# Performance work log

Hardware: AMD Instinct MI355X
Metric: run time of the kernel (lower is better)

The kernel has to match this reference:

```python
import jax, jax.numpy as jnp
import numpy as np

B, S, D_MODEL, D_K, D_V = 4, 2048, 1024, 1024, 1024


def setup_inputs() -> dict:
    key = jax.random.key(0)
    k1, k2, k3, k4 = jax.random.split(key, 4)
    scale = 1.0 / np.sqrt(D_MODEL)
    x = jax.random.normal(k1, (B, S, D_MODEL), dtype=jnp.float32)
    Wq = jax.random.normal(k2, (D_K, D_MODEL), dtype=jnp.float32) * scale
    Wk = jax.random.normal(k3, (D_K, D_MODEL), dtype=jnp.float32) * scale
    Wv = jax.random.normal(k4, (D_V, D_MODEL), dtype=jnp.float32) * scale
    # causal mask: position i may attend to j <= i (True = keep)
    mask = jnp.broadcast_to(jnp.tril(jnp.ones((S, S), dtype=bool)), (B, S, S))
    return {"x": x, "mask": mask, "Wq": Wq, "Wk": Wk, "Wv": Wv}


def reference(x, mask, Wq, Wk, Wv):
    # nn.Linear(d, k, bias=False): y = x @ W.T with W of shape [k, d]
    q = jnp.einsum('bsd,kd->bsk', x, Wq)
    k = jnp.einsum('bsd,kd->bsk', x, Wk)
    v = jnp.einsum('bsd,vd->bsv', x, Wv)
    scores = jnp.einsum('bik,bjk->bij', q, k) / jnp.sqrt(jnp.float32(D_K))
    s = jnp.where(mask, scores, -jnp.inf)
    # masked, fully-masked-row-safe softmax (fully masked rows -> all zeros,
    # matching softmax[all-masked rows] = 0 in the original)
    m = jnp.max(s, axis=-1, keepdims=True)
    m_safe = jnp.where(jnp.isfinite(m), m, 0.0)
    e = jnp.exp(s - m_safe)          # exp(-inf) = 0 for masked entries
    denom = jnp.sum(e, axis=-1, keepdims=True)
    p = e / jnp.where(denom == 0.0, 1.0, denom)
    return jnp.einsum('bij,bjv->biv', p, v)
```

## Files before the change

kernel.cpp:

```cpp
#include <hip/hip_runtime.h>
#include <hip/hip_bf16.h>
#include <stdint.h>

#define SEQ   2048
#define DM    1024
#define NBAT  4

typedef __attribute__((ext_vector_type(8))) short  short8;
typedef __attribute__((ext_vector_type(4))) float  floatx4;

__device__ __forceinline__ unsigned short f2b(float f) {
    __hip_bfloat16 h = __float2bfloat16(f);
    unsigned short r;
    __builtin_memcpy(&r, &h, 2);
    return r;
}

__device__ __forceinline__ ushort4 pack4(float a, float b, float c, float d) {
    ushort4 u; u.x = f2b(a); u.y = f2b(b); u.z = f2b(c); u.w = f2b(d); return u;
}

__device__ __forceinline__ void gload16(const void* g, void* s) {
    __builtin_amdgcn_global_load_lds(
        (const __attribute__((address_space(1))) unsigned int*)(uintptr_t)g,
        (__attribute__((address_space(3))) unsigned int*)(uintptr_t)s,
        16, 0, 0);
}

__global__ void prep(const float4* __restrict__ x,
                     const float4* __restrict__ w0, const float4* __restrict__ w1,
                     const float4* __restrict__ w2,
                     ushort4* __restrict__ xb, ushort4* __restrict__ wall,
                     float* __restrict__ rsum)
{
    const int b = blockIdx.x;
    const int t = threadIdx.x;
    if (b < 8192) {
        const int i = b * 256 + t;
        float4 f = x[i];
        xb[i] = pack4(f.x, f.y, f.z, f.w);
    } else if (b < 11264) {
        const int idx  = b - 8192;
        const int wsel = idx >> 10;
        const int i    = (idx & 1023) * 256 + t;
        const float4* src = (wsel == 0) ? w0 : (wsel == 1) ? w1 : w2;
        float4 f = src[i];
        wall[(size_t)wsel * 262144 + i] = pack4(f.x, f.y, f.z, f.w);
    } else {
        rsum[(b - 11264) * 256 + t] = 0.f;
    }
}

#define SLOTS 24576

__global__ __launch_bounds__(512, 2) void qkv_gemm(
    const unsigned short* __restrict__ A, const unsigned short* __restrict__ Bm,
    unsigned short* __restrict__ Qo, unsigned short* __restrict__ Ko,
    unsigned short* __restrict__ Vto, float qscale)
{
    __shared__ __align__(16) unsigned short lds[3 * SLOTS];

    const int bid = blockIdx.x;
    const int wg  = (bid & 7) * 96 + (bid >> 3);
    const int mt  = wg / 24, nt = wg - mt * 24;
    const int m0  = mt * 256, n0 = nt * 128;

    const int t    = threadIdx.x;
    const int w    = t >> 6;
    const int lane = t & 63;
    const int wr   = w >> 1, wc = w & 1;
    const int r    = lane & 15, q = lane >> 4;

    const int srow = lane >> 3;
    const int scol = ((lane & 7) ^ srow) << 3;

    const int aoff = (wr >> 1) * 8192 + ((wr & 1) * 64 + r) * 64;
    const int boff = 16384 + (wc * 64 + r) * 64;
    const int sk0  = ((0 + q) ^ (r & 7)) * 8;
    const int sk1  = ((4 + q) ^ (r & 7)) * 8;

    floatx4 acc[4][4];
#pragma unroll
    for (int i = 0; i < 4; i++)
#pragma unroll
        for (int j = 0; j < 4; j++)
            acc[i][j] = (floatx4){0.f, 0.f, 0.f, 0.f};

#define STGA(KB, SL) do { \
    gload16(A + (((size_t)(m0 +       w * 16 + srow)) << 10) + (KB) + scol, &lds[(SL) +         w * 1024]); \
    gload16(A + (((size_t)(m0 +   8 + w * 16 + srow)) << 10) + (KB) + scol, &lds[(SL) +         w * 1024 + 512]); \
    gload16(A + (((size_t)(m0 + 128 + w * 16 + srow)) << 10) + (KB) + scol, &lds[(SL) + 8192 +  w * 1024]); \
    gload16(A + (((size_t)(m0 + 136 + w * 16 + srow)) << 10) + (KB) + scol, &lds[(SL) + 8192 +  w * 1024 + 512]); \
  } while (0)
#define STGB(KB, SL) do { \
    gload16(Bm + (((size_t)(n0 +      w * 16 + srow)) << 10) + (KB) + scol, &lds[(SL) + 16384 + w * 1024]); \
    gload16(Bm + (((size_t)(n0 +  8 + w * 16 + srow)) << 10) + (KB) + scol, &lds[(SL) + 16384 + w * 1024 + 512]); \
  } while (0)

#define MFMA16() do { \
    acc[0][0] = __builtin_amdgcn_mfma_f32_16x16x32_bf16(af0, bf0, acc[0][0], 0, 0, 0); \
    acc[0][1] = __builtin_amdgcn_mfma_f32_16x16x32_bf16(af0, bf1, acc[0][1], 0, 0, 0); \
    acc[0][2] = __builtin_amdgcn_mfma_f32_16x16x32_bf16(af0, bf2, acc[0][2], 0, 0, 0); \
    acc[0][3] = __builtin_amdgcn_mfma_f32_16x16x32_bf16(af0, bf3, acc[0][3], 0, 0, 0); \
    acc[1][0] = __builtin_amdgcn_mfma_f32_16x16x32_bf16(af1, bf0, acc[1][0], 0, 0, 0); \
    acc[1][1] = __builtin_amdgcn_mfma_f32_16x16x32_bf16(af1, bf1, acc[1][1], 0, 0, 0); \
    acc[1][2] = __builtin_amdgcn_mfma_f32_16x16x32_bf16(af1, bf2, acc[1][2], 0, 0, 0); \
    acc[1][3] = __builtin_amdgcn_mfma_f32_16x16x32_bf16(af1, bf3, acc[1][3], 0, 0, 0); \
    acc[2][0] = __builtin_amdgcn_mfma_f32_16x16x32_bf16(af2, bf0, acc[2][0], 0, 0, 0); \
    acc[2][1] = __builtin_amdgcn_mfma_f32_16x16x32_bf16(af2, bf1, acc[2][1], 0, 0, 0); \
    acc[2][2] = __builtin_amdgcn_mfma_f32_16x16x32_bf16(af2, bf2, acc[2][2], 0, 0, 0); \
    acc[2][3] = __builtin_amdgcn_mfma_f32_16x16x32_bf16(af2, bf3, acc[2][3], 0, 0, 0); \
    acc[3][0] = __builtin_amdgcn_mfma_f32_16x16x32_bf16(af3, bf0, acc[3][0], 0, 0, 0); \
    acc[3][1] = __builtin_amdgcn_mfma_f32_16x16x32_bf16(af3, bf1, acc[3][1], 0, 0, 0); \
    acc[3][2] = __builtin_amdgcn_mfma_f32_16x16x32_bf16(af3, bf2, acc[3][2], 0, 0, 0); \
    acc[3][3] = __builtin_amdgcn_mfma_f32_16x16x32_bf16(af3, bf3, acc[3][3], 0, 0, 0); \
  } while (0)

    STGA(0, 0);
    STGB(0, 0);
    STGA(64, SLOTS);
    STGB(64, SLOTS);
    asm volatile("s_waitcnt vmcnt(6)" ::: "memory");
    __builtin_amdgcn_s_barrier();

    short8 af0, af1, af2, af3, bf0, bf1, bf2, bf3;

    for (int tt = 0; tt < 16; ++tt) {
        const int sl  = (tt % 3) * SLOTS;
        const int nsl = ((tt + 2) % 3) * SLOTS;
        const int nkb = (tt + 2 < 16) ? (tt + 2) * 64 : 0;

        {
            const int aB = sl + aoff + sk0;
            const int bB = sl + boff + sk0;
            af0 = *(const short8*)&lds[aB +    0];
            af1 = *(const short8*)&lds[aB + 1024];
            af2 = *(const short8*)&lds[aB + 2048];
            af3 = *(const short8*)&lds[aB + 3072];
            bf0 = *(const short8*)&lds[bB +    0];
            bf1 = *(const short8*)&lds[bB + 1024];
            bf2 = *(const short8*)&lds[bB + 2048];
            bf3 = *(const short8*)&lds[bB + 3072];
            STGA(nkb, nsl);
            __builtin_amdgcn_s_barrier();
            asm volatile("s_waitcnt lgkmcnt(0)" ::: "memory");
            __builtin_amdgcn_s_setprio(1);
            MFMA16();
            __builtin_amdgcn_s_setprio(0);
            __builtin_amdgcn_s_barrier();
        }
        {
            const int aB = sl + aoff + sk1;
            const int bB = sl + boff + sk1;
            af0 = *(const short8*)&lds[aB +    0];
            af1 = *(const short8*)&lds[aB + 1024];
            af2 = *(const short8*)&lds[aB + 2048];
            af3 = *(const short8*)&lds[aB + 3072];
            bf0 = *(const short8*)&lds[bB +    0];
            bf1 = *(const short8*)&lds[bB + 1024];
            bf2 = *(const short8*)&lds[bB + 2048];
            bf3 = *(const short8*)&lds[bB + 3072];
            STGB(nkb, nsl);
            asm volatile("s_waitcnt vmcnt(6)" ::: "memory");
            __builtin_amdgcn_s_barrier();
            asm volatile("s_waitcnt lgkmcnt(0)" ::: "memory");
            __builtin_amdgcn_s_setprio(1);
            MFMA16();
            __builtin_amdgcn_s_setprio(0);
            __builtin_amdgcn_s_barrier();
        }
    }
#undef STGA
#undef STGB
#undef MFMA16

    const int gmb = m0 + wr * 64 + q * 4;
    const int gnb = n0 + wc * 64 + r;
    if (nt < 8) {
#pragma unroll
        for (int i = 0; i < 4; i++) {
            const int gm = gmb + i * 16;
#pragma unroll
            for (int j = 0; j < 4; j++) {
                const int gn = gnb + j * 16;
#pragma unroll
                for (int rr = 0; rr < 4; rr++)
                    Qo[(size_t)(gm + rr) * 1024 + gn] = f2b(acc[i][j][rr] * qscale);
            }
        }
    } else if (nt < 16) {
#pragma unroll
        for (int i = 0; i < 4; i++) {
            const int gm = gmb + i * 16;
#pragma unroll
            for (int j = 0; j < 4; j++) {
                const int gn = gnb + j * 16;
#pragma unroll
                for (int rr = 0; rr < 4; rr++)
                    Ko[(size_t)(gm + rr) * 1024 + (gn - 1024)] = f2b(acc[i][j][rr]);
            }
        }
    } else {
#pragma unroll
        for (int i = 0; i < 4; i++) {
            const int gm = gmb + i * 16;
            const int b  = gm >> 11;
            const int s  = gm & 2047;
#pragma unroll
            for (int j = 0; j < 4; j++) {
                const int v = gnb + j * 16 - 2048;
                *(ushort4*)&Vto[((size_t)(b * 1024 + v)) * 2048 + s] =
                    pack4(acc[i][j][0], acc[i][j][1], acc[i][j][2], acc[i][j][3]);
            }
        }
    }
}

template<int MODE>
__global__ __launch_bounds__(512, 2) void attn256(
    const unsigned short* __restrict__ Ag, const unsigned short* __restrict__ Bg,
    void* __restrict__ Cv, float* __restrict__ rowsum)
{
    __shared__ __align__(16) unsigned short lds[3 * SLOTS];

    const int z = blockIdx.z;
    int m0, n0;
    if (MODE == 0) {
        const int f = blockIdx.x;
        int ti = (int)((sqrtf(4.f * f + 1.f) - 1.f) * 0.5f);
        while ((ti + 1) * (ti + 2) <= f) ti++;
        while (ti * (ti + 1) > f) ti--;
        const int tj = f - ti * (ti + 1);
        m0 = ti * 256;
        n0 = tj * 128;
    } else {
        m0 = (int)(gridDim.y - 1 - blockIdx.y) * 256;
        n0 = blockIdx.x * 128;
    }

    const size_t LDA = (MODE == 0) ? DM : SEQ;
    const size_t LDB = (MODE == 0) ? DM : SEQ;
    const unsigned short* A  = Ag + (size_t)z * ((MODE == 0) ? SEQ * DM : SEQ * SEQ);
    const unsigned short* Bm = Bg + (size_t)z * ((MODE == 0) ? SEQ * DM : DM * SEQ);
    const int NT = ((MODE == 0) ? DM : (m0 + 256)) / 64;

    const int t    = threadIdx.x;
    const int w    = t >> 6;
    const int lane = t & 63;
    const int wr   = w >> 1, wc = w & 1;
    const int r    = lane & 15, q = lane >> 4;

    const int srow = lane >> 3;
    const int scol = ((lane & 7) ^ srow) << 3;

    const int aoff = (wr >> 1) * 8192 + ((wr & 1) * 64 + r) * 64;
    const int boff = 16384 + (wc * 64 + r) * 64;
    const int sk0  = ((0 + q) ^ (r & 7)) * 8;
    const int sk1  = ((4 + q) ^ (r & 7)) * 8;

    floatx4 acc[4][4];
#pragma unroll
    for (int i = 0; i < 4; i++)
#pragma unroll
        for (int j = 0; j < 4; j++)
            acc[i][j] = (floatx4){0.f, 0.f, 0.f, 0.f};

#define ASTG(KB, SL) do { \
    gload16(A + (size_t)(m0 +       w * 16 + srow) * LDA + (KB) + scol, &lds[(SL) +         w * 1024]); \
    gload16(A + (size_t)(m0 +   8 + w * 16 + srow) * LDA + (KB) + scol, &lds[(SL) +         w * 1024 + 512]); \
    gload16(A + (size_t)(m0 + 128 + w * 16 + srow) * LDA + (KB) + scol, &lds[(SL) + 8192 +  w * 1024]); \
    gload16(A + (size_t)(m0 + 136 + w * 16 + srow) * LDA + (KB) + scol, &lds[(SL) + 8192 +  w * 1024 + 512]); \
  } while (0)
#define BSTG(KB, SL) do { \
    gload16(Bm + (size_t)(n0 +      w * 16 + srow) * LDB + (KB) + scol, &lds[(SL) + 16384 + w * 1024]); \
    gload16(Bm + (size_t)(n0 +  8 + w * 16 + srow) * LDB + (KB) + scol, &lds[(SL) + 16384 + w * 1024 + 512]); \
  } while (0)

#define MFMA16S() do { \
    acc[0][0] = __builtin_amdgcn_mfma_f32_16x16x32_bf16(bf0, af0, acc[0][0], 0, 0, 0); \
    acc[0][1] = __builtin_amdgcn_mfma_f32_16x16x32_bf16(bf1, af0, acc[0][1], 0, 0, 0); \
    acc[0][2] = __builtin_amdgcn_mfma_f32_16x16x32_bf16(bf2, af0, acc[0][2], 0, 0, 0); \
    acc[0][3] = __builtin_amdgcn_mfma_f32_16x16x32_bf16(bf3, af0, acc[0][3], 0, 0, 0); \
    acc[1][0] = __builtin_amdgcn_mfma_f32_16x16x32_bf16(bf0, af1, acc[1][0], 0, 0, 0); \
    acc[1][1] = __builtin_amdgcn_mfma_f32_16x16x32_bf16(bf1, af1, acc[1][1], 0, 0, 0); \
    acc[1][2] = __builtin_amdgcn_mfma_f32_16x16x32_bf16(bf2, af1, acc[1][2], 0, 0, 0); \
    acc[1][3] = __builtin_amdgcn_mfma_f32_16x16x32_bf16(bf3, af1, acc[1][3], 0, 0, 0); \
    acc[2][0] = __builtin_amdgcn_mfma_f32_16x16x32_bf16(bf0, af2, acc[2][0], 0, 0, 0); \
    acc[2][1] = __builtin_amdgcn_mfma_f32_16x16x32_bf16(bf1, af2, acc[2][1], 0, 0, 0); \
    acc[2][2] = __builtin_amdgcn_mfma_f32_16x16x32_bf16(bf2, af2, acc[2][2], 0, 0, 0); \
    acc[2][3] = __builtin_amdgcn_mfma_f32_16x16x32_bf16(bf3, af2, acc[2][3], 0, 0, 0); \
    acc[3][0] = __builtin_amdgcn_mfma_f32_16x16x32_bf16(bf0, af3, acc[3][0], 0, 0, 0); \
    acc[3][1] = __builtin_amdgcn_mfma_f32_16x16x32_bf16(bf1, af3, acc[3][1], 0, 0, 0); \
    acc[3][2] = __builtin_amdgcn_mfma_f32_16x16x32_bf16(bf2, af3, acc[3][2], 0, 0, 0); \
    acc[3][3] = __builtin_amdgcn_mfma_f32_16x16x32_bf16(bf3, af3, acc[3][3], 0, 0, 0); \
  } while (0)

    ASTG(0, 0);
    BSTG(0, 0);
    ASTG(64, SLOTS);
    BSTG(64, SLOTS);
    asm volatile("s_waitcnt vmcnt(6)" ::: "memory");
    __builtin_amdgcn_s_barrier();

    short8 af0, af1, af2, af3, bf0, bf1, bf2, bf3;

    for (int tt = 0; tt < NT; ++tt) {
        const int sl  = (tt % 3) * SLOTS;
        const int nsl = ((tt + 2) % 3) * SLOTS;
        const int nkb = (tt + 2 < NT) ? (tt + 2) * 64 : 0;

        {
            const int aB = sl + aoff + sk0;
            const int bB = sl + boff + sk0;
            af0 = *(const short8*)&lds[aB +    0];
            af1 = *(const short8*)&lds[aB + 1024];
            af2 = *(const short8*)&lds[aB + 2048];
            af3 = *(const short8*)&lds[aB + 3072];
            bf0 = *(const short8*)&lds[bB +    0];
            bf1 = *(const short8*)&lds[bB + 1024];
            bf2 = *(const short8*)&lds[bB + 2048];
            bf3 = *(const short8*)&lds[bB + 3072];
            ASTG(nkb, nsl);
            __builtin_amdgcn_s_barrier();
            asm volatile("s_waitcnt lgkmcnt(0)" ::: "memory");
            __builtin_amdgcn_s_setprio(1);
            MFMA16S();
            __builtin_amdgcn_s_setprio(0);
            __builtin_amdgcn_s_barrier();
        }
        {
            const int aB = sl + aoff + sk1;
            const int bB = sl + boff + sk1;
            af0 = *(const short8*)&lds[aB +    0];
            af1 = *(const short8*)&lds[aB + 1024];
            af2 = *(const short8*)&lds[aB + 2048];
            af3 = *(const short8*)&lds[aB + 3072];
            bf0 = *(const short8*)&lds[bB +    0];
            bf1 = *(const short8*)&lds[bB + 1024];
            bf2 = *(const short8*)&lds[bB + 2048];
            bf3 = *(const short8*)&lds[bB + 3072];
            BSTG(nkb, nsl);
            asm volatile("s_waitcnt vmcnt(6)" ::: "memory");
            __builtin_amdgcn_s_barrier();
            asm volatile("s_waitcnt lgkmcnt(0)" ::: "memory");
            __builtin_amdgcn_s_setprio(1);
            MFMA16S();
            __builtin_amdgcn_s_setprio(0);
            __builtin_amdgcn_s_barrier();
        }
    }
#undef ASTG
#undef BSTG
#undef MFMA16S

    const int gmb = m0 + wr * 64 + r;
    const int gnb = n0 + wc * 64 + q * 4;
    if (MODE == 0) {
        unsigned short* E = (unsigned short*)Cv + (size_t)z * SEQ * SEQ;
        float* rs = rowsum + (size_t)z * SEQ;
#pragma unroll
        for (int i = 0; i < 4; i++) {
            const int gm = gmb + i * 16;
            float part = 0.f;
#pragma unroll
            for (int j = 0; j < 4; j++) {
                const int gn = gnb + j * 16;
                float e0 = (gn + 0 <= gm) ? __expf(acc[i][j][0]) : 0.f;
                float e1 = (gn + 1 <= gm) ? __expf(acc[i][j][1]) : 0.f;
                float e2 = (gn + 2 <= gm) ? __expf(acc[i][j][2]) : 0.f;
                float e3 = (gn + 3 <= gm) ? __expf(acc[i][j][3]) : 0.f;
                part += (e0 + e1) + (e2 + e3);
                *(ushort4*)&E[(size_t)gm * SEQ + gn] = pack4(e0, e1, e2, e3);
            }
            part += __shfl_xor(part, 16, 64);
            part += __shfl_xor(part, 32, 64);
            if (q == 0) atomicAdd(&rs[gm], part);
        }
    } else {
        float* C = (float*)Cv + (size_t)z * SEQ * DM;
        const float* rs = rowsum + (size_t)z * SEQ;
#pragma unroll
        for (int i = 0; i < 4; i++) {
            const int gm = gmb + i * 16;
            const float inv = 1.0f / rs[gm];
#pragma unroll
            for (int j = 0; j < 4; j++) {
                const int gn = gnb + j * 16;
                float4 o;
                o.x = acc[i][j][0] * inv;
                o.y = acc[i][j][1] * inv;
                o.z = acc[i][j][2] * inv;
                o.w = acc[i][j][3] * inv;
                *(float4*)&C[(size_t)gm * DM + gn] = o;
            }
        }
    }
}

extern "C" void kernel_launch(void* const* d_in, const int* in_sizes, int n_in,
                              void* d_out, int out_size, void* d_ws, size_t ws_size,
                              hipStream_t stream) {
    (void)in_sizes; (void)n_in; (void)out_size; (void)ws_size;
    const float* x  = (const float*)d_in[0];
    const float* Wq = (const float*)d_in[2];
    const float* Wk = (const float*)d_in[3];
    const float* Wv = (const float*)d_in[4];

    char* base = (char*)d_ws;
    size_t off = 0;
    auto alloc = [&](size_t n) { char* p = base + off; off += (n + 255) & ~(size_t)255; return p; };

    unsigned short* xb   = (unsigned short*)alloc((size_t)NBAT * SEQ * DM * 2);
    unsigned short* wall = (unsigned short*)alloc((size_t)3 * DM * DM * 2);
    unsigned short* Qb   = (unsigned short*)alloc((size_t)NBAT * SEQ * DM * 2);
    unsigned short* Kb   = (unsigned short*)alloc((size_t)NBAT * SEQ * DM * 2);
    unsigned short* Vtb  = (unsigned short*)alloc((size_t)NBAT * DM * SEQ * 2);
    unsigned short* E    = (unsigned short*)alloc((size_t)NBAT * SEQ * SEQ * 2);
    float*          rsum = (float*)alloc((size_t)NBAT * SEQ * 4);

    prep<<<dim3(11296), dim3(256), 0, stream>>>(
        (const float4*)x, (const float4*)Wq, (const float4*)Wk, (const float4*)Wv,
        (ushort4*)xb, (ushort4*)wall, rsum);

    qkv_gemm<<<dim3(768), dim3(512), 0, stream>>>(
        xb, wall, Qb, Kb, Vtb, 0.03125f);

    attn256<0><<<dim3(72, 1, NBAT), dim3(512), 0, stream>>>(Qb, Kb, E, rsum);

    attn256<1><<<dim3(DM / 128, SEQ / 256, NBAT), dim3(512), 0, stream>>>(E, Vtb, d_out, rsum);
}
```

Baseline: 274.4 us.

## Merge two K half-steps per tile into one barrier-synchronised step

In both the projection GEMM and the scores GEMM, each 64-wide K tile used to run as two half-steps, each with its own LDS fragment loads, async global-to-LDS staging, several s_barriers and an lgkmcnt wait. Now each iteration loads all 16 fragments for both K halves at once, issues the A and B staging together, waits on vmcnt, takes a single barrier and runs 32 MFMAs back to back. This cuts barriers from four to one per tile and gives the scheduler a longer MFMA run to overlap with loads. In exchange it needs more VGPRs for the doubled fragments, which may lower occupancy. The wait that kept other waves from overwriting a slot still being read now depends only on the single barrier.

```diff
diff --git a/kernel.cpp b/kernel.cpp
--- a/kernel.cpp
+++ b/kernel.cpp
@@ -97,25 +97,6 @@
     gload16(Bm + (((size_t)(n0 +  8 + w * 16 + srow)) << 10) + (KB) + scol, &lds[(SL) + 16384 + w * 1024 + 512]); \
   } while (0)
 
-#define MFMA16() do { \
-    acc[0][0] = __builtin_amdgcn_mfma_f32_16x16x32_bf16(af0, bf0, acc[0][0], 0, 0, 0); \
-    acc[0][1] = __builtin_amdgcn_mfma_f32_16x16x32_bf16(af0, bf1, acc[0][1], 0, 0, 0); \
-    acc[0][2] = __builtin_amdgcn_mfma_f32_16x16x32_bf16(af0, bf2, acc[0][2], 0, 0, 0); \
-    acc[0][3] = __builtin_amdgcn_mfma_f32_16x16x32_bf16(af0, bf3, acc[0][3], 0, 0, 0); \
-    acc[1][0] = __builtin_amdgcn_mfma_f32_16x16x32_bf16(af1, bf0, acc[1][0], 0, 0, 0); \
-    acc[1][1] = __builtin_amdgcn_mfma_f32_16x16x32_bf16(af1, bf1, acc[1][1], 0, 0, 0); \
-    acc[1][2] = __builtin_amdgcn_mfma_f32_16x16x32_bf16(af1, bf2, acc[1][2], 0, 0, 0); \
-    acc[1][3] = __builtin_amdgcn_mfma_f32_16x16x32_bf16(af1, bf3, acc[1][3], 0, 0, 0); \
-    acc[2][0] = __builtin_amdgcn_mfma_f32_16x16x32_bf16(af2, bf0, acc[2][0], 0, 0, 0); \
-    acc[2][1] = __builtin_amdgcn_mfma_f32_16x16x32_bf16(af2, bf1, acc[2][1], 0, 0, 0); \
-    acc[2][2] = __builtin_amdgcn_mfma_f32_16x16x32_bf16(af2, bf2, acc[2][2], 0, 0, 0); \
-    acc[2][3] = __builtin_amdgcn_mfma_f32_16x16x32_bf16(af2, bf3, acc[2][3], 0, 0, 0); \
-    acc[3][0] = __builtin_amdgcn_mfma_f32_16x16x32_bf16(af3, bf0, acc[3][0], 0, 0, 0); \
-    acc[3][1] = __builtin_amdgcn_mfma_f32_16x16x32_bf16(af3, bf1, acc[3][1], 0, 0, 0); \
-    acc[3][2] = __builtin_amdgcn_mfma_f32_16x16x32_bf16(af3, bf2, acc[3][2], 0, 0, 0); \
-    acc[3][3] = __builtin_amdgcn_mfma_f32_16x16x32_bf16(af3, bf3, acc[3][3], 0, 0, 0); \
-  } while (0)
-
     STGA(0, 0);
     STGB(0, 0);
     STGA(64, SLOTS);
@@ -123,56 +104,72 @@
     asm volatile("s_waitcnt vmcnt(6)" ::: "memory");
     __builtin_amdgcn_s_barrier();
 
-    short8 af0, af1, af2, af3, bf0, bf1, bf2, bf3;
-
     for (int tt = 0; tt < 16; ++tt) {
         const int sl  = (tt % 3) * SLOTS;
         const int nsl = ((tt + 2) % 3) * SLOTS;
         const int nkb = (tt + 2 < 16) ? (tt + 2) * 64 : 0;
 
-        {
-            const int aB = sl + aoff + sk0;
-            const int bB = sl + boff + sk0;
-            af0 = *(const short8*)&lds[aB +    0];
-            af1 = *(const short8*)&lds[aB + 1024];
-            af2 = *(const short8*)&lds[aB + 2048];
-            af3 = *(const short8*)&lds[aB + 3072];
-            bf0 = *(const short8*)&lds[bB +    0];
-            bf1 = *(const short8*)&lds[bB + 1024];
-            bf2 = *(const short8*)&lds[bB + 2048];
-            bf3 = *(const short8*)&lds[bB + 3072];
-            STGA(nkb, nsl);
-            __builtin_amdgcn_s_barrier();
-            asm volatile("s_waitcnt lgkmcnt(0)" ::: "memory");
-            __builtin_amdgcn_s_setprio(1);
-            MFMA16();
-            __builtin_amdgcn_s_setprio(0);
-            __builtin_amdgcn_s_barrier();
-        }
-        {
-            const int aB = sl + aoff + sk1;
-            const int bB = sl + boff + sk1;
-            af0 = *(const short8*)&lds[aB +    0];
-            af1 = *(const short8*)&lds[aB + 1024];
-            af2 = *(const short8*)&lds[aB + 2048];
-            af3 = *(const short8*)&lds[aB + 3072];
-            bf0 = *(const short8*)&lds[bB +    0];
-            bf1 = *(const short8*)&lds[bB + 1024];
-            bf2 = *(const short8*)&lds[bB + 2048];
-            bf3 = *(const short8*)&lds[bB + 3072];
-            STGB(nkb, nsl);
-            asm volatile("s_waitcnt vmcnt(6)" ::: "memory");
-            __builtin_amdgcn_s_barrier();
-            asm volatile("s_waitcnt lgkmcnt(0)" ::: "memory");
-            __builtin_amdgcn_s_setprio(1);
-            MFMA16();
-            __builtin_amdgcn_s_setprio(0);
-            __builtin_amdgcn_s_barrier();
-        }
+        const int aB = sl + aoff;
+        const int bB = sl + boff;
+        short8 a00 = *(const short8*)&lds[aB + sk0 +    0];
+        short8 a10 = *(const short8*)&lds[aB + sk0 + 1024];
+        short8 a20 = *(const short8*)&lds[aB + sk0 + 2048];
+        short8 a30 = *(const short8*)&lds[aB + sk0 + 3072];
+        short8 b00 = *(const short8*)&lds[bB + sk0 +    0];
+        short8 b10 = *(const short8*)&lds[bB + sk0 + 1024];
+        short8 b20 = *(const short8*)&lds[bB + sk0 + 2048];
+        short8 b30 = *(const short8*)&lds[bB + sk0 + 3072];
+        short8 a01 = *(const short8*)&lds[aB + sk1 +    0];
+        short8 a11 = *(const short8*)&lds[aB + sk1 + 1024];
+        short8 a21 = *(const short8*)&lds[aB + sk1 + 2048];
+        short8 a31 = *(const short8*)&lds[aB + sk1 + 3072];
+        short8 b01 = *(const short8*)&lds[bB + sk1 +    0];
+        short8 b11 = *(const short8*)&lds[bB + sk1 + 1024];
+        short8 b21 = *(const short8*)&lds[bB + sk1 + 2048];
+        short8 b31 = *(const short8*)&lds[bB + sk1 + 3072];
+
+        STGA(nkb, nsl);
+        STGB(nkb, nsl);
+        asm volatile("s_waitcnt vmcnt(6)" ::: "memory");
+        __builtin_amdgcn_s_barrier();
+
+        __builtin_amdgcn_s_setprio(1);
+        acc[0][0] = __builtin_amdgcn_mfma_f32_16x16x32_bf16(a00, b00, acc[0][0], 0, 0, 0);
+        acc[0][1] = __builtin_amdgcn_mfma_f32_16x16x32_bf16(a00, b10, acc[0][1], 0, 0, 0);
+        acc[0][2] = __builtin_amdgcn_mfma_f32_16x16x32_bf16(a00, b20, acc[0][2], 0, 0, 0);
+        acc[0][3] = __builtin_amdgcn_mfma_f32_16x16x32_bf16(a00, b30, acc[0][3], 0, 0, 0);
+        acc[1][0] = __builtin_amdgcn_mfma_f32_16x16x32_bf16(a10, b00, acc[1][0], 0, 0, 0);
+        acc[1][1] = __builtin_amdgcn_mfma_f32_16x16x32_bf16(a10, b10, acc[1][1], 0, 0, 0);
+        acc[1][2] = __builtin_amdgcn_mfma_f32_16x16x32_bf16(a10, b20, acc[1][2], 0, 0, 0);
+        acc[1][3] = __builtin_amdgcn_mfma_f32_16x16x32_bf16(a10, b30, acc[1][3], 0, 0, 0);
+        acc[2][0] = __builtin_amdgcn_mfma_f32_16x16x32_bf16(a20, b00, acc[2][0], 0, 0, 0);
+        acc[2][1] = __builtin_amdgcn_mfma_f32_16x16x32_bf16(a20, b10, acc[2][1], 0, 0, 0);
+        acc[2][2] = __builtin_amdgcn_mfma_f32_16x16x32_bf16(a20, b20, acc[2][2], 0, 0, 0);
+        acc[2][3] = __builtin_amdgcn_mfma_f32_16x16x32_bf16(a20, b30, acc[2][3], 0, 0, 0);
+        acc[3][0] = __builtin_amdgcn_mfma_f32_16x16x32_bf16(a30, b00, acc[3][0], 0, 0, 0);
+        acc[3][1] = __builtin_amdgcn_mfma_f32_16x16x32_bf16(a30, b10, acc[3][1], 0, 0, 0);
+        acc[3][2] = __builtin_amdgcn_mfma_f32_16x16x32_bf16(a30, b20, acc[3][2], 0, 0, 0);
+        acc[3][3] = __builtin_amdgcn_mfma_f32_16x16x32_bf16(a30, b30, acc[3][3], 0, 0, 0);
+        acc[0][0] = __builtin_amdgcn_mfma_f32_16x16x32_bf16(a01, b01, acc[0][0], 0, 0, 0);
+        acc[0][1] = __builtin_amdgcn_mfma_f32_16x16x32_bf16(a01, b11, acc[0][1], 0, 0, 0);
+        acc[0][2] = __builtin_amdgcn_mfma_f32_16x16x32_bf16(a01, b21, acc[0][2], 0, 0, 0);
+        acc[0][3] = __builtin_amdgcn_mfma_f32_16x16x32_bf16(a01, b31, acc[0][3], 0, 0, 0);
+        acc[1][0] = __builtin_amdgcn_mfma_f32_16x16x32_bf16(a11, b01, acc[1][0], 0, 0, 0);
+        acc[1][1] = __builtin_amdgcn_mfma_f32_16x16x32_bf16(a11, b11, acc[1][1], 0, 0, 0);
+        acc[1][2] = __builtin_amdgcn_mfma_f32_16x16x32_bf16(a11, b21, acc[1][2], 0, 0, 0);
+        acc[1][3] = __builtin_amdgcn_mfma_f32_16x16x32_bf16(a11, b31, acc[1][3], 0, 0, 0);
+        acc[2][0] = __builtin_amdgcn_mfma_f32_16x16x32_bf16(a21, b01, acc[2][0], 0, 0, 0);
+        acc[2][1] = __builtin_amdgcn_mfma_f32_16x16x32_bf16(a21, b11, acc[2][1], 0, 0, 0);
+        acc[2][2] = __builtin_amdgcn_mfma_f32_16x16x32_bf16(a21, b21, acc[2][2], 0, 0, 0);
+        acc[2][3] = __builtin_amdgcn_mfma_f32_16x16x32_bf16(a21, b31, acc[2][3], 0, 0, 0);
+        acc[3][0] = __builtin_amdgcn_mfma_f32_16x16x32_bf16(a31, b01, acc[3][0], 0, 0, 0);
+        acc[3][1] = __builtin_amdgcn_mfma_f32_16x16x32_bf16(a31, b11, acc[3][1], 0, 0, 0);
+        acc[3][2] = __builtin_amdgcn_mfma_f32_16x16x32_bf16(a31, b21, acc[3][2], 0, 0, 0);
+        acc[3][3] = __builtin_amdgcn_mfma_f32_16x16x32_bf16(a31, b31, acc[3][3], 0, 0, 0);
+        __builtin_amdgcn_s_setprio(0);
     }
 #undef STGA
 #undef STGB
-#undef MFMA16
 
     const int gmb = m0 + wr * 64 + q * 4;
     const int gnb = n0 + wc * 64 + r;
@@ -276,25 +273,6 @@
     gload16(Bm + (size_t)(n0 +  8 + w * 16 + srow) * LDB + (KB) + scol, &lds[(SL) + 16384 + w * 1024 + 512]); \
   } while (0)
 
-#define MFMA16S() do { \
-    acc[0][0] = __builtin_amdgcn_mfma_f32_16x16x32_bf16(bf0, af0, acc[0][0], 0, 0, 0); \
-    acc[0][1] = __builtin_amdgcn_mfma_f32_16x16x32_bf16(bf1, af0, acc[0][1], 0, 0, 0); \
-    acc[0][2] = __builtin_amdgcn_mfma_f32_16x16x32_bf16(bf2, af0, acc[0][2], 0, 0, 0); \
-    acc[0][3] = __builtin_amdgcn_mfma_f32_16x16x32_bf16(bf3, af0, acc[0][3], 0, 0, 0); \
-    acc[1][0] = __builtin_amdgcn_mfma_f32_16x16x32_bf16(bf0, af1, acc[1][0], 0, 0, 0); \
-    acc[1][1] = __builtin_amdgcn_mfma_f32_16x16x32_bf16(bf1, af1, acc[1][1], 0, 0, 0); \
-    acc[1][2] = __builtin_amdgcn_mfma_f32_16x16x32_bf16(bf2, af1, acc[1][2], 0, 0, 0); \
-    acc[1][3] = __builtin_amdgcn_mfma_f32_16x16x32_bf16(bf3, af1, acc[1][3], 0, 0, 0); \
-    acc[2][0] = __builtin_amdgcn_mfma_f32_16x16x32_bf16(bf0, af2, acc[2][0], 0, 0, 0); \
-    acc[2][1] = __builtin_amdgcn_mfma_f32_16x16x32_bf16(bf1, af2, acc[2][1], 0, 0, 0); \
-    acc[2][2] = __builtin_amdgcn_mfma_f32_16x16x32_bf16(bf2, af2, acc[2][2], 0, 0, 0); \
-    acc[2][3] = __builtin_amdgcn_mfma_f32_16x16x32_bf16(bf3, af2, acc[2][3], 0, 0, 0); \
-    acc[3][0] = __builtin_amdgcn_mfma_f32_16x16x32_bf16(bf0, af3, acc[3][0], 0, 0, 0); \
-    acc[3][1] = __builtin_amdgcn_mfma_f32_16x16x32_bf16(bf1, af3, acc[3][1], 0, 0, 0); \
-    acc[3][2] = __builtin_amdgcn_mfma_f32_16x16x32_bf16(bf2, af3, acc[3][2], 0, 0, 0); \
-    acc[3][3] = __builtin_amdgcn_mfma_f32_16x16x32_bf16(bf3, af3, acc[3][3], 0, 0, 0); \
-  } while (0)
-
     ASTG(0, 0);
     BSTG(0, 0);
     ASTG(64, SLOTS);
@@ -302,56 +280,72 @@
     asm volatile("s_waitcnt vmcnt(6)" ::: "memory");
     __builtin_amdgcn_s_barrier();
 
-    short8 af0, af1, af2, af3, bf0, bf1, bf2, bf3;
-
     for (int tt = 0; tt < NT; ++tt) {
         const int sl  = (tt % 3) * SLOTS;
         const int nsl = ((tt + 2) % 3) * SLOTS;
         const int nkb = (tt + 2 < NT) ? (tt + 2) * 64 : 0;
 
-        {
-            const int aB = sl + aoff + sk0;
-            const int bB = sl + boff + sk0;
-            af0 = *(const short8*)&lds[aB +    0];
-            af1 = *(const short8*)&lds[aB + 1024];
-            af2 = *(const short8*)&lds[aB + 2048];
-            af3 = *(const short8*)&lds[aB + 3072];
-            bf0 = *(const short8*)&lds[bB +    0];
-            bf1 = *(const short8*)&lds[bB + 1024];
-            bf2 = *(const short8*)&lds[bB + 2048];
-            bf3 = *(const short8*)&lds[bB + 3072];
-            ASTG(nkb, nsl);
-            __builtin_amdgcn_s_barrier();
-            asm volatile("s_waitcnt lgkmcnt(0)" ::: "memory");
-            __builtin_amdgcn_s_setprio(1);
-            MFMA16S();
-            __builtin_amdgcn_s_setprio(0);
-            __builtin_amdgcn_s_barrier();
-        }
-        {
-            const int aB = sl + aoff + sk1;
-            const int bB = sl + boff + sk1;
-            af0 = *(const short8*)&lds[aB +    0];
-            af1 = *(const short8*)&lds[aB + 1024];
-            af2 = *(const short8*)&lds[aB + 2048];
-            af3 = *(const short8*)&lds[aB + 3072];
-            bf0 = *(const short8*)&lds[bB +    0];
-            bf1 = *(const short8*)&lds[bB + 1024];
-            bf2 = *(const short8*)&lds[bB + 2048];
-            bf3 = *(const short8*)&lds[bB + 3072];
-            BSTG(nkb, nsl);
-            asm volatile("s_waitcnt vmcnt(6)" ::: "memory");
-            __builtin_amdgcn_s_barrier();
-            asm volatile("s_waitcnt lgkmcnt(0)" ::: "memory");
-            __builtin_amdgcn_s_setprio(1);
-            MFMA16S();
-            __builtin_amdgcn_s_setprio(0);
-            __builtin_amdgcn_s_barrier();
-        }
+        const int aB = sl + aoff;
+        const int bB = sl + boff;
+        short8 a00 = *(const short8*)&lds[aB + sk0 +    0];
+        short8 a10 = *(const short8*)&lds[aB + sk0 + 1024];
+        short8 a20 = *(const short8*)&lds[aB + sk0 + 2048];
+        short8 a30 = *(const short8*)&lds[aB + sk0 + 3072];
+        short8 b00 = *(const short8*)&lds[bB + sk0 +    0];
+        short8 b10 = *(const short8*)&lds[bB + sk0 + 1024];
+        short8 b20 = *(const short8*)&lds[bB + sk0 + 2048];
+        short8 b30 = *(const short8*)&lds[bB + sk0 + 3072];
+        short8 a01 = *(const short8*)&lds[aB + sk1 +    0];
+        short8 a11 = *(const short8*)&lds[aB + sk1 + 1024];
+        short8 a21 = *(const short8*)&lds[aB + sk1 + 2048];
+        short8 a31 = *(const short8*)&lds[aB + sk1 + 3072];
+        short8 b01 = *(const short8*)&lds[bB + sk1 +    0];
+        short8 b11 = *(const short8*)&lds[bB + sk1 + 1024];
+        short8 b21 = *(const short8*)&lds[bB + sk1 + 2048];
+        short8 b31 = *(const short8*)&lds[bB + sk1 + 3072];
+
+        ASTG(nkb, nsl);
+        BSTG(nkb, nsl);
+        asm volatile("s_waitcnt vmcnt(6)" ::: "memory");
+        __builtin_amdgcn_s_barrier();
+
+        __builtin_amdgcn_s_setprio(1);
+        acc[0][0] = __builtin_amdgcn_mfma_f32_16x16x32_bf16(b00, a00, acc[0][0], 0, 0, 0);
+        acc[0][1] = __builtin_amdgcn_mfma_f32_16x16x32_bf16(b10, a00, acc[0][1], 0, 0, 0);
+        acc[0][2] = __builtin_amdgcn_mfma_f32_16x16x32_bf16(b20, a00, acc[0][2], 0, 0, 0);
+        acc[0][3] = __builtin_amdgcn_mfma_f32_16x16x32_bf16(b30, a00, acc[0][3], 0, 0, 0);
+        acc[1][0] = __builtin_amdgcn_mfma_f32_16x16x32_bf16(b00, a10, acc[1][0], 0, 0, 0);
+        acc[1][1] = __builtin_amdgcn_mfma_f32_16x16x32_bf16(b10, a10, acc[1][1], 0, 0, 0);
+        acc[1][2] = __builtin_amdgcn_mfma_f32_16x16x32_bf16(b20, a10, acc[1][2], 0, 0, 0);
+        acc[1][3] = __builtin_amdgcn_mfma_f32_16x16x32_bf16(b30, a10, acc[1][3], 0, 0, 0);
+        acc[2][0] = __builtin_amdgcn_mfma_f32_16x16x32_bf16(b00, a20, acc[2][0], 0, 0, 0);
+        acc[2][1] = __builtin_amdgcn_mfma_f32_16x16x32_bf16(b10, a20, acc[2][1], 0, 0, 0);
+        acc[2][2] = __builtin_amdgcn_mfma_f32_16x16x32_bf16(b20, a20, acc[2][2], 0, 0, 0);
+        acc[2][3] = __builtin_amdgcn_mfma_f32_16x16x32_bf16(b30, a20, acc[2][3], 0, 0, 0);
+        acc[3][0] = __builtin_amdgcn_mfma_f32_16x16x32_bf16(b00, a30, acc[3][0], 0, 0, 0);
+        acc[3][1] = __builtin_amdgcn_mfma_f32_16x16x32_bf16(b10, a30, acc[3][1], 0, 0, 0);
+        acc[3][2] = __builtin_amdgcn_mfma_f32_16x16x32_bf16(b20, a30, acc[3][2], 0, 0, 0);
+        acc[3][3] = __builtin_amdgcn_mfma_f32_16x16x32_bf16(b30, a30, acc[3][3], 0, 0, 0);
+        acc[0][0] = __builtin_amdgcn_mfma_f32_16x16x32_bf16(b01, a01, acc[0][0], 0, 0, 0);
+        acc[0][1] = __builtin_amdgcn_mfma_f32_16x16x32_bf16(b11, a01, acc[0][1], 0, 0, 0);
+        acc[0][2] = __builtin_amdgcn_mfma_f32_16x16x32_bf16(b21, a01, acc[0][2], 0, 0, 0);
+        acc[0][3] = __builtin_amdgcn_mfma_f32_16x16x32_bf16(b31, a01, acc[0][3], 0, 0, 0);
+        acc[1][0] = __builtin_amdgcn_mfma_f32_16x16x32_bf16(b01, a11, acc[1][0], 0, 0, 0);
+        acc[1][1] = __builtin_amdgcn_mfma_f32_16x16x32_bf16(b11, a11, acc[1][1], 0, 0, 0);
+        acc[1][2] = __builtin_amdgcn_mfma_f32_16x16x32_bf16(b21, a11, acc[1][2], 0, 0, 0);
+        acc[1][3] = __builtin_amdgcn_mfma_f32_16x16x32_bf16(b31, a11, acc[1][3], 0, 0, 0);
+        acc[2][0] = __builtin_amdgcn_mfma_f32_16x16x32_bf16(b01, a21, acc[2][0], 0, 0, 0);
+        acc[2][1] = __builtin_amdgcn_mfma_f32_16x16x32_bf16(b11, a21, acc[2][1], 0, 0, 0);
+        acc[2][2] = __builtin_amdgcn_mfma_f32_16x16x32_bf16(b21, a21, acc[2][2], 0, 0, 0);
+        acc[2][3] = __builtin_amdgcn_mfma_f32_16x16x32_bf16(b31, a21, acc[2][3], 0, 0, 0);
+        acc[3][0] = __builtin_amdgcn_mfma_f32_16x16x32_bf16(b01, a31, acc[3][0], 0, 0, 0);
+        acc[3][1] = __builtin_amdgcn_mfma_f32_16x16x32_bf16(b11, a31, acc[3][1], 0, 0, 0);
+        acc[3][2] = __builtin_amdgcn_mfma_f32_16x16x32_bf16(b21, a31, acc[3][2], 0, 0, 0);
+        acc[3][3] = __builtin_amdgcn_mfma_f32_16x16x32_bf16(b31, a31, acc[3][3], 0, 0, 0);
+        __builtin_amdgcn_s_setprio(0);
     }
 #undef ASTG
 #undef BSTG
-#undef MFMA16S
 
     const int gmb = m0 + wr * 64 + r;
     const int gnb = n0 + wc * 64 + q * 4;
```

Result: faster. 260.5 us (-5.1%).
